# Optimization experiments

Measured on AMD Instinct MI355X. Metric: run time of the kernel, lower is better.

Reference implementation:

```python
import jax, jax.numpy as jnp
import numpy as np

N_NODES = 100000
N_EDGES = 1600000
D_IN = 32
D_OUT = 32


def setup_inputs() -> dict:
    key = jax.random.key(0)
    ks = jax.random.split(key, 5)
    feat = jax.random.normal(ks[0], (N_NODES, D_IN), dtype=jnp.float32)
    # xavier_uniform with relu gain, shape (out, in)
    gain = float(np.sqrt(2.0))
    bound = gain * float(np.sqrt(6.0 / (D_IN + D_OUT)))
    W_self = jax.random.uniform(ks[1], (D_OUT, D_IN), minval=-bound, maxval=bound, dtype=jnp.float32)
    W_neigh = jax.random.uniform(ks[2], (D_OUT, D_IN), minval=-bound, maxval=bound, dtype=jnp.float32)
    b_neigh = jnp.zeros((D_OUT,), dtype=jnp.float32)
    src = jax.random.randint(ks[3], (N_EDGES,), 0, N_NODES)
    dst = jax.random.randint(ks[4], (N_EDGES,), 0, N_NODES)
    return {"feat": feat, "W_self": W_self, "W_neigh": W_neigh,
            "b_neigh": b_neigh, "src": src, "dst": dst}


def reference(feat, W_self, W_neigh, b_neigh, src, dst):
    # copy_src + mean aggregation: gather src features, segment-sum into dst,
    # divide by in-degree (0 for isolated dst nodes, matching DGL mean).
    msgs = feat[src]  # [E, D_in] irregular gather
    neigh_sum = jax.ops.segment_sum(msgs, dst, num_segments=N_NODES)  # [N, D_in]
    deg = jax.ops.segment_sum(jnp.ones((dst.shape[0],), feat.dtype), dst,
                              num_segments=N_NODES)  # [N]
    neigh = neigh_sum / jnp.maximum(deg, 1.0)[:, None]
    # GraphSAGE combine: fc_self(h_self) + fc_neigh(neigh)
    rst = feat @ W_self.T + neigh @ W_neigh.T + b_neigh
    return rst
```

## Files before the change

### kernel.cpp

```cpp
#include <hip/hip_runtime.h>

#define D 32
#define SHIFT 7
#define P 128
#define BMAX 1024
#define TILE 4096
#define STHREADS 1024
#define CAP 3072
#define TMAX 512
#define AP 37
#define WP 36

#define FXS 131072.0f
#define FXINV 7.62939453125e-06f

__global__ __launch_bounds__(STHREADS) void scatter_tiles(
        const int* __restrict__ src, const int* __restrict__ dst,
        int* __restrict__ records, int* __restrict__ starts, int E, int Bn) {
    __shared__ int lhist[STHREADS];
    __shared__ int lofs[BMAX];
    __shared__ int wsum[16];

    int t = threadIdx.x;
    int lane = t & 63;
    int wid = t >> 6;
    int tileStart = blockIdx.x * TILE;

    lhist[t] = 0;
    __syncthreads();

    int sarr[4], darr[4];
    int e0 = tileStart + 4 * t;
    if (tileStart + TILE <= E) {
        int4 s4 = ((const int4*)src)[tileStart / 4 + t];
        int4 d4 = ((const int4*)dst)[tileStart / 4 + t];
        sarr[0] = s4.x; sarr[1] = s4.y; sarr[2] = s4.z; sarr[3] = s4.w;
        darr[0] = d4.x; darr[1] = d4.y; darr[2] = d4.z; darr[3] = d4.w;
    } else {
#pragma unroll
        for (int i = 0; i < 4; ++i) {
            int e = e0 + i;
            sarr[i] = (e < E) ? src[e] : 0;
            darr[i] = (e < E) ? dst[e] : 0;
        }
    }

    int recs[4], bks[4], rr[4];
#pragma unroll
    for (int i = 0; i < 4; ++i) {
        int e = e0 + i;
        if (e < E) {
            int b = darr[i] >> SHIFT;
            recs[i] = (sarr[i] << SHIFT) | (darr[i] & (P - 1));
            bks[i] = b;
            rr[i] = atomicAdd(&lhist[b], 1);
        } else bks[i] = -1;
    }
    __syncthreads();

    int own = lhist[t];
    int v = own;
#pragma unroll
    for (int off = 1; off < 64; off <<= 1) {
        int u = __shfl_up(v, off, 64);
        if (lane >= off) v += u;
    }
    if (lane == 63) wsum[wid] = v;
    __syncthreads();
    if (wid == 0) {
        int s = (lane < 16) ? wsum[lane] : 0;
#pragma unroll
        for (int off = 1; off < 16; off <<= 1) {
            int u = __shfl_up(s, off, 64);
            if (lane >= off) s += u;
        }
        if (lane < 16) wsum[lane] = s;
    }
    __syncthreads();
    int incl = v + (wid ? wsum[wid - 1] : 0);
    int ex = incl - own;
    if (t <= Bn) starts[(size_t)blockIdx.x * (Bn + 1) + t] = ex;
    if (t < Bn) lofs[t] = ex;
    __syncthreads();

#pragma unroll
    for (int i = 0; i < 4; ++i) {
        if (bks[i] >= 0)
            records[tileStart + lofs[bks[i]] + rr[i]] = recs[i];
    }
}

__global__ __launch_bounds__(256) void transpose_starts(
        const int* __restrict__ s, int* __restrict__ sT, int T, int C) {
    __shared__ int tile[32][33];
    int r0 = blockIdx.x * 32, c0 = blockIdx.y * 32;
    int tx = threadIdx.x & 31, ty = threadIdx.x >> 5;
    for (int dy = ty; dy < 32; dy += 8) {
        int r = r0 + dy, c = c0 + tx;
        tile[dy][tx] = (r < T && c < C) ? s[(size_t)r * C + c] : 0;
    }
    __syncthreads();
    for (int dy = ty; dy < 32; dy += 8) {
        int c = c0 + dy, r = r0 + tx;
        if (c < C && r < T) sT[(size_t)c * T + r] = tile[tx][dy];
    }
}

__global__ __launch_bounds__(512) void bucket_final(
        const float* __restrict__ feat, const int* __restrict__ records,
        const int* __restrict__ startsT,
        const float* __restrict__ Wself, const float* __restrict__ Wneigh,
        const float* __restrict__ bias, float* __restrict__ out,
        int N, int T, int Bn) {
    __shared__ float4 ubuf[1024];
    __shared__ int sacc[P * AP];
    __shared__ float sWs[D * WP];
    __shared__ float sWn[D * WP];
    __shared__ float sb[D];
    __shared__ int sdeg[P];
    __shared__ int tstart[TMAX];
    __shared__ int tbase[TMAX + 1];
    __shared__ int wsum2[8];

    int* raw = reinterpret_cast<int*>(ubuf);
    float* sfeatF = reinterpret_cast<float*>(ubuf);
    float* saccF = reinterpret_cast<float*>(sacc);

    int b = blockIdx.x;
    int t = threadIdx.x;
    int lane = t & 63;
    int wid = t >> 6;

    float4 fr0 = make_float4(0.f, 0.f, 0.f, 0.f);
    float4 fr1 = fr0;
    {
        int n0 = (b << SHIFT) + (t >> 3);
        int n1 = (b << SHIFT) + ((t + 512) >> 3);
        if (n0 < N) fr0 = ((const float4*)feat)[(size_t)n0 * 8 + (t & 7)];
        if (n1 < N) fr1 = ((const float4*)feat)[(size_t)n1 * 8 + (t & 7)];
    }

    for (int i = t; i < P * AP; i += 512) sacc[i] = 0;
    if (t < P) sdeg[t] = 0;
    for (int i = t; i < D * D; i += 512) {
        int r = i >> 5, c = i & 31;
        sWs[r * WP + c] = Wself[i];
        sWn[r * WP + c] = Wneigh[i];
    }
    if (t < D) sb[t] = bias[t];

    int myc = 0;
    if (t < T) {
        int s0v = startsT[(size_t)b * T + t];
        int s1v = startsT[(size_t)(b + 1) * T + t];
        tstart[t] = s0v;
        myc = s1v - s0v;
    }
    int v = myc;
#pragma unroll
    for (int off = 1; off < 64; off <<= 1) {
        int u = __shfl_up(v, off, 64);
        if (lane >= off) v += u;
    }
    if (lane == 63) wsum2[wid] = v;
    __syncthreads();
    if (wid == 0) {
        int s = (lane < 8) ? wsum2[lane] : 0;
#pragma unroll
        for (int off = 1; off < 8; off <<= 1) {
            int u = __shfl_up(s, off, 64);
            if (lane >= off) s += u;
        }
        if (lane < 8) wsum2[lane] = s;
    }
    __syncthreads();
    int incl = v + (wid ? wsum2[wid - 1] : 0);
    if (t < T) tbase[t] = incl - myc;
    if (t == T - 1) tbase[T] = incl;
    __syncthreads();

    int m = min(tbase[T], CAP);

    int lane4 = t & 3, tg4 = t >> 2;
    for (int tau = tg4; tau < T; tau += 128) {
        int s = tstart[tau];
        int rb = tbase[tau];
        int c2 = tbase[tau + 1] - rb;
        const int* rp = records + (size_t)tau * TILE + s;
        for (int l = lane4; l < c2; l += 4) {
            int pos = rb + l;
            if (pos < CAP) raw[pos] = rp[l];
        }
    }
    __syncthreads();

    int team = t >> 3;
    int part = t & 7;
    for (int base = team; base < m; base += 256) {
        float4 vv[4];
        int nl8[4];
        bool ok[4];
#pragma unroll
        for (int u = 0; u < 4; ++u) {
            int idx = base + 64 * u;
            ok[u] = idx < m;
            int rec = raw[ok[u] ? idx : 0];
            int s = rec >> SHIFT;
            nl8[u] = rec & (P - 1);
            vv[u] = *reinterpret_cast<const float4*>(
                feat + (size_t)s * D + part * 4);
        }
#pragma unroll
        for (int u = 0; u < 4; ++u) {
            if (ok[u]) {
                int* ac = &sacc[nl8[u] * AP + part * 4];
                atomicAdd(ac + 0, __float2int_rn(vv[u].x * FXS));
                atomicAdd(ac + 1, __float2int_rn(vv[u].y * FXS));
                atomicAdd(ac + 2, __float2int_rn(vv[u].z * FXS));
                atomicAdd(ac + 3, __float2int_rn(vv[u].w * FXS));
                if (part == 0) atomicAdd(&sdeg[nl8[u]], 1);
            }
        }
    }
    __syncthreads();

    int rv[8];
#pragma unroll
    for (int r = 0; r < 8; ++r) {
        int i = t + 512 * r;
        rv[r] = sacc[(i >> 5) * AP + (i & 31)];
    }
    __syncthreads();
#pragma unroll
    for (int r = 0; r < 8; ++r) {
        int i = t + 512 * r;
        saccF[i] = (float)rv[r] * FXINV;
    }
    ubuf[t] = fr0;
    ubuf[t + 512] = fr1;
    __syncthreads();

    int j = t & 31;
    int nb = t >> 5;
    const float4* wsr = reinterpret_cast<const float4*>(&sWs[j * WP]);
    const float4* wnr = reinterpret_cast<const float4*>(&sWn[j * WP]);
    float bj = sb[j];
#pragma unroll
    for (int q = 0; q < 8; ++q) {
        int nl = q * 16 + nb;
        int n = (b << SHIFT) + nl;
        if (n >= N) continue;
        const float4* fr = reinterpret_cast<const float4*>(&sfeatF[nl * 32]);
        const float4* nr = reinterpret_cast<const float4*>(&saccF[nl * 32]);
        float accS = 0.f, accN = 0.f;
#pragma unroll
        for (int kk = 0; kk < 8; ++kk) {
            float4 f4 = fr[kk], w4 = wsr[kk];
            accS += f4.x * w4.x + f4.y * w4.y + f4.z * w4.z + f4.w * w4.w;
            float4 n4 = nr[kk], u4 = wnr[kk];
            accN += n4.x * u4.x + n4.y * u4.y + n4.z * u4.z + n4.w * u4.w;
        }
        float inv = 1.0f / (float)max(sdeg[nl], 1);
        out[(size_t)n * D + j] = accS + inv * accN + bj;
    }
}

extern "C" void kernel_launch(void* const* d_in, const int* in_sizes, int n_in,
                              void* d_out, int out_size, void* d_ws, size_t ws_size,
                              hipStream_t stream) {
    const float* feat   = (const float*)d_in[0];
    const float* Wself  = (const float*)d_in[1];
    const float* Wneigh = (const float*)d_in[2];
    const float* bnb    = (const float*)d_in[3];
    const int*   src    = (const int*)d_in[4];
    const int*   dst    = (const int*)d_in[5];

    int N = in_sizes[0] / D;
    int E = in_sizes[4];
    int Bn = (N + P - 1) / P;
    int T  = (E + TILE - 1) / TILE;
    int C  = Bn + 1;

    int* records = (int*)d_ws;
    int* starts  = records + (size_t)T * TILE;
    int* startsT = starts + (size_t)T * C;

    scatter_tiles<<<T, STHREADS, 0, stream>>>(src, dst, records, starts, E, Bn);
    dim3 tg((T + 31) / 32, (C + 31) / 32);
    transpose_starts<<<tg, 256, 0, stream>>>(starts, startsT, T, C);
    bucket_final<<<Bn, 512, 0, stream>>>(feat, records, startsT, Wself, Wneigh, bnb,
                                         (float*)d_out, N, T, Bn);
}
```

Measured before the change: 144.1 us.

## Drop transpose kernel, stage records in LDS, deepen gather unroll

The scatter kernel now writes bucket start offsets directly in transposed layout, so the separate transpose kernel and its launch are gone. Records are first placed into a shared-memory staging buffer and then written out with coalesced int4 stores instead of scattered global writes. The gather loop in the final kernel issues eight feature loads per thread instead of four to keep more memory requests in flight. The costs are extra LDS use in the scatter kernel, strided global writes for the transposed starts, and more registers in the gather loop.

```diff
diff --git a/kernel.cpp b/kernel.cpp
--- a/kernel.cpp
+++ b/kernel.cpp
@@ -16,10 +16,11 @@
 
 __global__ __launch_bounds__(STHREADS) void scatter_tiles(
         const int* __restrict__ src, const int* __restrict__ dst,
-        int* __restrict__ records, int* __restrict__ starts, int E, int Bn) {
+        int* __restrict__ records, int* __restrict__ startsT, int E, int Bn, int T) {
     __shared__ int lhist[STHREADS];
     __shared__ int lofs[BMAX];
     __shared__ int wsum[16];
+    __shared__ int stage[TILE];
 
     int t = threadIdx.x;
     int lane = t & 63;
@@ -79,31 +80,19 @@
     __syncthreads();
     int incl = v + (wid ? wsum[wid - 1] : 0);
     int ex = incl - own;
-    if (t <= Bn) starts[(size_t)blockIdx.x * (Bn + 1) + t] = ex;
+    if (t <= Bn) startsT[(size_t)t * T + blockIdx.x] = ex;
     if (t < Bn) lofs[t] = ex;
     __syncthreads();
 
 #pragma unroll
     for (int i = 0; i < 4; ++i) {
-        if (bks[i] >= 0)
-            records[tileStart + lofs[bks[i]] + rr[i]] = recs[i];
-    }
-}
-
-__global__ __launch_bounds__(256) void transpose_starts(
-        const int* __restrict__ s, int* __restrict__ sT, int T, int C) {
-    __shared__ int tile[32][33];
-    int r0 = blockIdx.x * 32, c0 = blockIdx.y * 32;
-    int tx = threadIdx.x & 31, ty = threadIdx.x >> 5;
-    for (int dy = ty; dy < 32; dy += 8) {
-        int r = r0 + dy, c = c0 + tx;
-        tile[dy][tx] = (r < T && c < C) ? s[(size_t)r * C + c] : 0;
-    }
-    __syncthreads();
-    for (int dy = ty; dy < 32; dy += 8) {
-        int c = c0 + dy, r = r0 + tx;
-        if (c < C && r < T) sT[(size_t)c * T + r] = tile[tx][dy];
-    }
+        if (bks[i] >= 0) stage[lofs[bks[i]] + rr[i]] = recs[i];
+    }
+    __syncthreads();
+
+    int4* dp = reinterpret_cast<int4*>(records + (size_t)tileStart);
+    const int4* sp = reinterpret_cast<const int4*>(stage);
+    dp[t] = sp[t];
 }
 
 __global__ __launch_bounds__(512) void bucket_final(
@@ -196,12 +185,12 @@
 
     int team = t >> 3;
     int part = t & 7;
-    for (int base = team; base < m; base += 256) {
-        float4 vv[4];
-        int nl8[4];
-        bool ok[4];
-#pragma unroll
-        for (int u = 0; u < 4; ++u) {
+    for (int base = team; base < m; base += 512) {
+        float4 vv[8];
+        int nl8[8];
+        bool ok[8];
+#pragma unroll
+        for (int u = 0; u < 8; ++u) {
             int idx = base + 64 * u;
             ok[u] = idx < m;
             int rec = raw[ok[u] ? idx : 0];
@@ -211,7 +200,7 @@
                 feat + (size_t)s * D + part * 4);
         }
 #pragma unroll
-        for (int u = 0; u < 4; ++u) {
+        for (int u = 0; u < 8; ++u) {
             if (ok[u]) {
                 int* ac = &sacc[nl8[u] * AP + part * 4];
                 atomicAdd(ac + 0, __float2int_rn(vv[u].x * FXS));
@@ -279,15 +268,11 @@
     int E = in_sizes[4];
     int Bn = (N + P - 1) / P;
     int T  = (E + TILE - 1) / TILE;
-    int C  = Bn + 1;
 
     int* records = (int*)d_ws;
-    int* starts  = records + (size_t)T * TILE;
-    int* startsT = starts + (size_t)T * C;
-
-    scatter_tiles<<<T, STHREADS, 0, stream>>>(src, dst, records, starts, E, Bn);
-    dim3 tg((T + 31) / 32, (C + 31) / 32);
-    transpose_starts<<<tg, 256, 0, stream>>>(starts, startsT, T, C);
+    int* startsT = records + (size_t)T * TILE;
+
+    scatter_tiles<<<T, STHREADS, 0, stream>>>(src, dst, records, startsT, E, Bn, T);
     bucket_final<<<Bn, 512, 0, stream>>>(feat, records, startsT, Wself, Wneigh, bnb,
                                          (float*)d_out, N, T, Bn);
 }
```

Measured after the change: 135.0 us. 1.07x faster.
